# Optimization experiments

Measured on AMD Instinct MI355X. Metric: run time of the kernel, lower is better.

## Reference

```python
import jax, jax.numpy as jnp
import numpy as np

HEADS = 8


def setup_inputs() -> dict:
    key = jax.random.key(0)
    ks = jax.random.split(key, 6)
    B, N, D = 4, 2048, 512
    return {
        "x": jax.random.normal(ks[0], (B, N, D), dtype=jnp.float32),
        "pos": jax.random.uniform(ks[1], (B, N, 3), dtype=jnp.float32),
        "qkv_w": jax.random.normal(ks[2], (3 * D, D), dtype=jnp.float32) * 0.02,
        "qkv_b": jax.random.normal(ks[3], (3 * D,), dtype=jnp.float32) * 0.02,
        "out_w": jax.random.normal(ks[4], (D, D), dtype=jnp.float32) * 0.02,
        "out_b": jax.random.normal(ks[5], (D,), dtype=jnp.float32) * 0.02,
    }


def reference(x, pos, qkv_w, qkv_b, out_w, out_b):
    B, N, D = x.shape
    H = HEADS
    Dh = D // H
    scale = D ** (-0.5)  # NOTE: original uses full dim, not head dim

    # QKV projection -> [3, B, H, N, Dh]
    qkv = (x @ qkv_w.T + qkv_b).reshape(B, N, 3, H, Dh).transpose(2, 0, 3, 1, 4)
    q, k, v = qkv[0], qkv[1], qkv[2]

    # partial 3D RoPE on first 6 head dims (3 axis pairs)
    theta = pos * jnp.pi                    # [B, N, 3]
    sin = jnp.sin(theta)[:, None]           # [B, 1, N, 3] broadcasts over heads
    cos = jnp.cos(theta)[:, None]

    def rotate(t):
        x_rot = t[..., :6]
        x1 = x_rot[..., 0::2]               # [B, H, N, 3]
        x2 = x_rot[..., 1::2]
        return jnp.concatenate(
            [x1 * cos - x2 * sin, x1 * sin + x2 * cos, t[..., 6:]], axis=-1
        )

    q = rotate(q)
    k = rotate(k)

    attn = jax.nn.softmax(jnp.einsum("bhqd,bhkd->bhqk", q, k) * scale, axis=-1)
    out = jnp.einsum("bhqk,bhkd->bhqd", attn, v)          # [B, H, N, Dh]
    out = out.transpose(0, 2, 1, 3).reshape(B, N, D)
    return out @ out_w.T + out_b
```

## Files before the change

### kernel.cpp

```cpp
#include <hip/hip_runtime.h>
#include <stdint.h>

typedef __attribute__((ext_vector_type(4))) float f32x4;
typedef __attribute__((ext_vector_type(16))) float f32x16;
typedef __attribute__((ext_vector_type(8))) short bf16x8;
typedef __attribute__((ext_vector_type(4))) unsigned short u16x4;

__device__ __forceinline__ unsigned short f2bf(float f) {
    unsigned int u = __builtin_bit_cast(unsigned int, f);
    u += 0x7fffu + ((u >> 16) & 1u);
    return (unsigned short)(u >> 16);
}
__device__ __forceinline__ float bf2f(unsigned short s) {
    unsigned int u = ((unsigned int)s) << 16;
    return __builtin_bit_cast(float, u);
}
__device__ __forceinline__ float fexp2(float x) {
#if __has_builtin(__builtin_amdgcn_exp2f)
    return __builtin_amdgcn_exp2f(x);
#else
    return exp2f(x);
#endif
}
__device__ __forceinline__ unsigned int cvt_pk_bf16(float lo, float hi) {
    unsigned int r;
    asm("v_cvt_pk_bf16_f32 %0, %1, %2" : "=v"(r) : "v"(lo), "v"(hi));
    return r;
}

__global__ void k_cvt3(const float* __restrict__ x,
                       const float* __restrict__ w1,
                       const float* __restrict__ w2,
                       unsigned short* __restrict__ out) {
    const int C1 = 1048576;
    const int C2 = 196608;
    int i = blockIdx.x * blockDim.x + threadIdx.x;
    f32x4 v;
    if (i < C1)            v = ((const f32x4*)x)[i];
    else if (i < C1 + C2)  v = ((const f32x4*)w1)[i - C1];
    else                   v = ((const f32x4*)w2)[i - C1 - C2];
    u16x4 o;
    o.x = f2bf(v.x); o.y = f2bf(v.y); o.z = f2bf(v.z); o.w = f2bf(v.w);
    ((u16x4*)out)[i] = o;
}

template<int OUT_BF16>
__global__ __launch_bounds__(256, 2)
void k_gemm_nt(const unsigned short* __restrict__ A,
               const unsigned short* __restrict__ Bm,
               const float* __restrict__ bias,
               void* __restrict__ Cout, int M, int N, int K) {
    __shared__ unsigned short As[2][128 * 64];
    __shared__ unsigned short Bs[2][128 * 64];
    const int tid = threadIdx.x;
    const int lane = tid & 63;
    const int w = tid >> 6;
    const int wr = (w >> 1) * 64, wc = (w & 1) * 64;
    const int g = lane >> 4, fr = lane & 15;

    f32x4 acc[4][4];
#pragma unroll
    for (int i = 0; i < 4; ++i)
#pragma unroll
        for (int j = 0; j < 4; ++j) acc[i][j] = f32x4{0.f, 0.f, 0.f, 0.f};

    const int srow8 = lane >> 3;
    const int swc = ((lane & 7) ^ srow8) * 8;
    const unsigned short* Abase = A + (size_t)(blockIdx.x * 128 + w * 8 + srow8) * K + swc;
    const unsigned short* Bbase = Bm + (size_t)(blockIdx.y * 128 + w * 8 + srow8) * K + swc;

    auto stage = [&](int bsel, int k0) {
        char* ldsA = (char*)&As[bsel][0] + w * 1024;
        char* ldsB = (char*)&Bs[bsel][0] + w * 1024;
#pragma unroll
        for (int i = 0; i < 4; ++i) {
            __builtin_amdgcn_global_load_lds(
                (const __attribute__((address_space(1))) void*)(Abase + (size_t)i * 32 * K + k0),
                (__attribute__((address_space(3))) void*)(ldsA + i * 4096), 16, 0, 0);
            __builtin_amdgcn_global_load_lds(
                (const __attribute__((address_space(1))) void*)(Bbase + (size_t)i * 32 * K + k0),
                (__attribute__((address_space(3))) void*)(ldsB + i * 4096), 16, 0, 0);
        }
    };
    auto compute = [&](int bsel) {
        bf16x8 af[2][4], bfv[2][4];
#pragma unroll
        for (int kk = 0; kk < 2; ++kk) {
#pragma unroll
            for (int mi = 0; mi < 4; ++mi)
                af[kk][mi] = *(const bf16x8*)&As[bsel][(wr + mi * 16 + fr) * 64 + (((kk * 4 + g) ^ (fr & 7)) * 8)];
#pragma unroll
            for (int ni = 0; ni < 4; ++ni)
                bfv[kk][ni] = *(const bf16x8*)&Bs[bsel][(wc + ni * 16 + fr) * 64 + (((kk * 4 + g) ^ (fr & 7)) * 8)];
        }
        __builtin_amdgcn_s_setprio(1);
#pragma unroll
        for (int kk = 0; kk < 2; ++kk)
#pragma unroll
            for (int mi = 0; mi < 4; ++mi)
#pragma unroll
                for (int ni = 0; ni < 4; ++ni)
                    acc[mi][ni] = __builtin_amdgcn_mfma_f32_16x16x32_bf16(af[kk][mi], bfv[kk][ni], acc[mi][ni], 0, 0, 0);
        __builtin_amdgcn_s_setprio(0);
    };

    const int nt = K >> 6;
    stage(0, 0);
    int cur = 0;
#pragma unroll 1
    for (int t = 0; t < nt - 1; ++t) {
        __builtin_amdgcn_s_barrier();
        stage(cur ^ 1, (t + 1) << 6);
        asm volatile("s_waitcnt vmcnt(8)" ::: "memory");
        __builtin_amdgcn_s_barrier();
        compute(cur);
        cur ^= 1;
    }
    asm volatile("s_waitcnt vmcnt(0)" ::: "memory");
    __builtin_amdgcn_s_barrier();
    compute(cur);

#pragma unroll
    for (int mi = 0; mi < 4; ++mi) {
#pragma unroll
        for (int ni = 0; ni < 4; ++ni) {
            int row = blockIdx.x * 128 + wr + mi * 16 + g * 4;
            int col = blockIdx.y * 128 + wc + ni * 16 + fr;
            float bz = bias[col];
#pragma unroll
            for (int r = 0; r < 4; ++r) {
                float v = acc[mi][ni][r] + bz;
                if (OUT_BF16) ((unsigned short*)Cout)[(size_t)(row + r) * N + col] = f2bf(v);
                else          ((float*)Cout)[(size_t)(row + r) * N + col] = v;
            }
        }
    }
}

__global__ void k_rotary(const unsigned short* __restrict__ qkv,
                         const float* __restrict__ pos,
                         unsigned short* __restrict__ Qb,
                         unsigned short* __restrict__ Kb,
                         unsigned short* __restrict__ VT) {
    const float PI = 3.14159265358979323846f;
    const float QS = 0.04419417382415922f * 1.44269504088896341f;
    int cid = blockIdx.x * 256 + threadIdx.x;
    int s = cid >> 19;
    int r = cid & 524287;
    if (s < 2) {
        int m = r >> 6, c = r & 63;
        int h = c >> 3, dc = c & 7;
        int b = m >> 11, n = m & 2047;
        bf16x8 v = *(const bf16x8*)&qkv[m * 1536 + s * 512 + c * 8];
        float f[8];
#pragma unroll
        for (int i = 0; i < 8; ++i) f[i] = bf2f((unsigned short)v[i]);
        if (dc == 0) {
            float nf[6];
#pragma unroll
            for (int j = 0; j < 3; ++j) {
                float th = pos[m * 3 + j] * PI;
                float sn = __sinf(th), cs = __cosf(th);
                float x1 = f[2 * j], x2 = f[2 * j + 1];
                nf[j] = x1 * cs - x2 * sn;
                nf[3 + j] = x1 * sn + x2 * cs;
            }
#pragma unroll
            for (int j = 0; j < 6; ++j) f[j] = nf[j];
        }
        if (s == 0) {
#pragma unroll
            for (int i = 0; i < 8; ++i) f[i] *= QS;
        }
        bf16x8 o;
#pragma unroll
        for (int i = 0; i < 8; ++i) o[i] = (short)f2bf(f[i]);
        unsigned short* dst = (s == 0) ? Qb : Kb;
        *(bf16x8*)&dst[((size_t)(b * 8 + h) * 2048 + n) * 64 + dc * 8] = o;
    } else {
        int cd = r >> 13;
        int m = r & 8191;
        int b = m >> 11, n = m & 2047;
        int h = cd >> 3, d8 = (cd & 7) * 8;
        bf16x8 v = *(const bf16x8*)&qkv[m * 1536 + 1024 + cd * 8];
        int q2 = (n >> 2) & 3;
        int np = n + (q2 == 1 ? 4 : (q2 == 2 ? -4 : 0));
        size_t base = ((size_t)(b * 8 + h) * 64 + d8) * 2048 + np;
#pragma unroll
        for (int i = 0; i < 8; ++i) VT[base + (size_t)i * 2048] = (unsigned short)v[i];
    }
}

__global__ __launch_bounds__(512, 4)
void k_attn(const unsigned short* __restrict__ Qb,
            const unsigned short* __restrict__ Kb,
            const unsigned short* __restrict__ VT,
            unsigned short* __restrict__ Ob) {
    __shared__ unsigned short smem[2][2][2][4096];
    const int tid = threadIdx.x, lane = tid & 63, w = tid >> 6;
    const int wl = w & 3, half = w >> 2;
    const int l31 = lane & 31, hi = lane >> 5;
    const int bid = blockIdx.x;
    const int bh = (bid & 7) * 4 + ((bid >> 3) >> 4);
    const int qb = (bid >> 3) & 15;
    const int b = bh >> 3, h = bh & 7;
    const int qr0 = qb * 128 + wl * 32;
    const unsigned short* Q = Qb + (size_t)bh * 2048 * 64;
    const unsigned short* K = Kb + (size_t)bh * 2048 * 64;
    const unsigned short* V = VT + (size_t)bh * 64 * 2048;
    const int thalf = half * 16;

    const int srow8 = lane >> 3;
    const int swc = ((lane & 7) ^ srow8) << 3;
    const int sA = wl, sB = wl + 4;

    bf16x8 bq[4];
#pragma unroll
    for (int ds = 0; ds < 4; ++ds)
        bq[ds] = *(const bf16x8*)&Q[(size_t)(qr0 + l31) * 64 + ds * 16 + hi * 8];

    f32x16 oT0, oT1;
#pragma unroll
    for (int i = 0; i < 16; ++i) { oT0[i] = 0.f; oT1[i] = 0.f; }
    float lpart = 0.f;

    auto stage = [&](int bsel, int t) {
        const int kv0 = t * 64;
        const unsigned short* k0 = K + (size_t)(kv0 + sA * 8 + srow8) * 64 + swc;
        const unsigned short* k1 = K + (size_t)(kv0 + sB * 8 + srow8) * 64 + swc;
        const unsigned short* v0 = V + (size_t)(sA * 8 + srow8) * 2048 + kv0 + swc;
        const unsigned short* v1 = V + (size_t)(sB * 8 + srow8) * 2048 + kv0 + swc;
        char* dk = (char*)&smem[half][0][bsel][0];
        char* dv = (char*)&smem[half][1][bsel][0];
        __builtin_amdgcn_global_load_lds((const __attribute__((address_space(1))) void*)k0,
                                         (__attribute__((address_space(3))) void*)(dk + sA * 1024), 16, 0, 0);
        __builtin_amdgcn_global_load_lds((const __attribute__((address_space(1))) void*)k1,
                                         (__attribute__((address_space(3))) void*)(dk + sB * 1024), 16, 0, 0);
        __builtin_amdgcn_global_load_lds((const __attribute__((address_space(1))) void*)v0,
                                         (__attribute__((address_space(3))) void*)(dv + sA * 1024), 16, 0, 0);
        __builtin_amdgcn_global_load_lds((const __attribute__((address_space(1))) void*)v1,
                                         (__attribute__((address_space(3))) void*)(dv + sB * 1024), 16, 0, 0);
    };

    auto pack8 = [&](const float* p) -> bf16x8 {
        union { unsigned int u[4]; bf16x8 v; } c;
        c.u[0] = cvt_pk_bf16(p[0], p[1]);
        c.u[1] = cvt_pk_bf16(p[2], p[3]);
        c.u[2] = cvt_pk_bf16(p[4], p[5]);
        c.u[3] = cvt_pk_bf16(p[6], p[7]);
        return c.v;
    };

    auto compute = [&](int bsel) {
        const unsigned short* KsC = &smem[half][0][bsel][0];
        const unsigned short* VtC = &smem[half][1][bsel][0];
        f32x16 s0, s1;
#pragma unroll
        for (int i = 0; i < 16; ++i) { s0[i] = 0.f; s1[i] = 0.f; }
        __builtin_amdgcn_s_setprio(1);
#pragma unroll
        for (int ds = 0; ds < 4; ++ds) {
            const int c = ((((ds << 1) | hi) ^ (l31 & 7)) << 3);
            bf16x8 ka0 = *(const bf16x8*)&KsC[l31 * 64 + c];
            bf16x8 ka1 = *(const bf16x8*)&KsC[(32 + l31) * 64 + c];
            s0 = __builtin_amdgcn_mfma_f32_32x32x16_bf16(ka0, bq[ds], s0, 0, 0, 0);
            s1 = __builtin_amdgcn_mfma_f32_32x32x16_bf16(ka1, bq[ds], s1, 0, 0, 0);
        }
        __builtin_amdgcn_s_setprio(0);
        float p0[16], p1[16];
        float lsum = 0.f;
#pragma unroll
        for (int r = 0; r < 16; ++r) {
            p0[r] = fexp2(s0[r]);
            p1[r] = fexp2(s1[r]);
            lsum += p0[r] + p1[r];
        }
        lpart += lsum;
        bf16x8 pb0 = pack8(p0);
        bf16x8 pb1 = pack8(p0 + 8);
        bf16x8 pb2 = pack8(p1);
        bf16x8 pb3 = pack8(p1 + 8);
        __builtin_amdgcn_s_setprio(1);
#pragma unroll
        for (int kb = 0; kb < 4; ++kb) {
            const int c = ((((kb << 1) | hi) ^ (l31 & 7)) << 3);
            bf16x8 av0 = *(const bf16x8*)&VtC[l31 * 64 + c];
            bf16x8 av1 = *(const bf16x8*)&VtC[(32 + l31) * 64 + c];
            bf16x8 pbk = (kb == 0) ? pb0 : (kb == 1) ? pb1 : (kb == 2) ? pb2 : pb3;
            oT0 = __builtin_amdgcn_mfma_f32_32x32x16_bf16(av0, pbk, oT0, 0, 0, 0);
            oT1 = __builtin_amdgcn_mfma_f32_32x32x16_bf16(av1, pbk, oT1, 0, 0, 0);
        }
        __builtin_amdgcn_s_setprio(0);
    };

    stage(0, thalf);
    int cur = 0;
#pragma unroll 1
    for (int t = 0; t < 15; ++t) {
        __builtin_amdgcn_s_barrier();
        stage(cur ^ 1, thalf + t + 1);
        asm volatile("s_waitcnt vmcnt(4)" ::: "memory");
        __builtin_amdgcn_s_barrier();
        compute(cur);
        cur ^= 1;
    }
    asm volatile("s_waitcnt vmcnt(0)" ::: "memory");
    __builtin_amdgcn_s_barrier();
    compute(cur);

    __syncthreads();
    float* mrg = (float*)&smem[0][0][0][0];
    float* slot = mrg + (size_t)(wl * 64 + lane) * 33;
    if (half) {
#pragma unroll
        for (int i = 0; i < 16; ++i) { slot[i] = oT0[i]; slot[16 + i] = oT1[i]; }
        slot[32] = lpart;
    }
    __syncthreads();
    if (!half) {
#pragma unroll
        for (int i = 0; i < 16; ++i) { oT0[i] += slot[i]; oT1[i] += slot[16 + i]; }
        float lf = lpart + slot[32];
        lf += __shfl_xor(lf, 32, 64);
        float il = 1.f / lf;
        size_t rowbase = (size_t)(b * 2048 + qr0 + l31) * 512 + h * 64;
#pragma unroll
        for (int grp = 0; grp < 4; ++grp) {
            u16x4 o0, o1;
#pragma unroll
            for (int i = 0; i < 4; ++i) {
                o0[i] = f2bf(oT0[grp * 4 + i] * il);
                o1[i] = f2bf(oT1[grp * 4 + i] * il);
            }
            int dv0 = grp * 8 + 4 * hi;
            *(u16x4*)&Ob[rowbase + dv0] = o0;
            *(u16x4*)&Ob[rowbase + 32 + dv0] = o1;
        }
    }
}

extern "C" void kernel_launch(void* const* d_in, const int* in_sizes, int n_in,
                              void* d_out, int out_size, void* d_ws, size_t ws_size,
                              hipStream_t stream) {
    const float* x     = (const float*)d_in[0];
    const float* pos   = (const float*)d_in[1];
    const float* qkv_w = (const float*)d_in[2];
    const float* qkv_b = (const float*)d_in[3];
    const float* out_w = (const float*)d_in[4];
    const float* out_b = (const float*)d_in[5];
    float* out = (float*)d_out;

    unsigned short* Xb   = (unsigned short*)d_ws;
    unsigned short* W1b  = Xb   + (size_t)8192 * 512;
    unsigned short* W2b  = W1b  + (size_t)1536 * 512;
    unsigned short* QKVb = W2b  + (size_t)512 * 512;
    unsigned short* Qb   = QKVb + (size_t)8192 * 1536;
    unsigned short* Kb   = Qb   + (size_t)4194304;
    unsigned short* VTb  = Kb   + (size_t)4194304;
    unsigned short* Ob   = VTb  + (size_t)4194304;

    k_cvt3<<<5120, 256, 0, stream>>>(x, qkv_w, out_w, Xb);
    k_gemm_nt<1><<<dim3(64, 12), 256, 0, stream>>>(Xb, W1b, qkv_b, QKVb, 8192, 1536, 512);
    k_rotary<<<6144, 256, 0, stream>>>(QKVb, pos, Qb, Kb, VTb);
    k_attn<<<512, 512, 0, stream>>>(Qb, Kb, VTb, Ob);
    k_gemm_nt<0><<<dim3(64, 4), 256, 0, stream>>>(Ob, W2b, out_b, out, 8192, 512, 512);
}
```

Baseline: 96.03 us.

## Restructure GEMM and attention pipelines to one barrier per step with smaller K tiles

The GEMM kernel halves its K tile from 64 to 32, shrinking LDS buffers and using a 4-chunk XOR swizzle. Both the GEMM and attention loops move from a two-barrier-per-iteration scheme, which waited on loads before computing, to a single barrier per step. The next tile is issued, the current one is computed, and only then does the loop wait and synchronize, so loads overlap a full compute step. The trade-off is more loop iterations and barriers per K, with less MFMA work between them.

```diff
diff --git a/kernel.cpp b/kernel.cpp
--- a/kernel.cpp
+++ b/kernel.cpp
@@ -50,8 +50,8 @@
                const unsigned short* __restrict__ Bm,
                const float* __restrict__ bias,
                void* __restrict__ Cout, int M, int N, int K) {
-    __shared__ unsigned short As[2][128 * 64];
-    __shared__ unsigned short Bs[2][128 * 64];
+    __shared__ unsigned short As[2][128 * 32];
+    __shared__ unsigned short Bs[2][128 * 32];
     const int tid = threadIdx.x;
     const int lane = tid & 63;
     const int w = tid >> 6;
@@ -64,61 +64,59 @@
 #pragma unroll
         for (int j = 0; j < 4; ++j) acc[i][j] = f32x4{0.f, 0.f, 0.f, 0.f};
 
-    const int srow8 = lane >> 3;
-    const int swc = ((lane & 7) ^ srow8) * 8;
-    const unsigned short* Abase = A + (size_t)(blockIdx.x * 128 + w * 8 + srow8) * K + swc;
-    const unsigned short* Bbase = Bm + (size_t)(blockIdx.y * 128 + w * 8 + srow8) * K + swc;
+    const int srow16 = lane >> 2;
+    const int schunk = ((lane & 3) ^ (srow16 & 3)) * 8;
+    const int sA = w, sB = w + 4;
+    const unsigned short* Aseg0 = A + (size_t)(blockIdx.x * 128 + sA * 16 + srow16) * K + schunk;
+    const unsigned short* Aseg1 = A + (size_t)(blockIdx.x * 128 + sB * 16 + srow16) * K + schunk;
+    const unsigned short* Bseg0 = Bm + (size_t)(blockIdx.y * 128 + sA * 16 + srow16) * K + schunk;
+    const unsigned short* Bseg1 = Bm + (size_t)(blockIdx.y * 128 + sB * 16 + srow16) * K + schunk;
 
     auto stage = [&](int bsel, int k0) {
-        char* ldsA = (char*)&As[bsel][0] + w * 1024;
-        char* ldsB = (char*)&Bs[bsel][0] + w * 1024;
-#pragma unroll
-        for (int i = 0; i < 4; ++i) {
-            __builtin_amdgcn_global_load_lds(
-                (const __attribute__((address_space(1))) void*)(Abase + (size_t)i * 32 * K + k0),
-                (__attribute__((address_space(3))) void*)(ldsA + i * 4096), 16, 0, 0);
-            __builtin_amdgcn_global_load_lds(
-                (const __attribute__((address_space(1))) void*)(Bbase + (size_t)i * 32 * K + k0),
-                (__attribute__((address_space(3))) void*)(ldsB + i * 4096), 16, 0, 0);
-        }
+        char* la = (char*)&As[bsel][0];
+        char* lb = (char*)&Bs[bsel][0];
+        __builtin_amdgcn_global_load_lds((const __attribute__((address_space(1))) void*)(Aseg0 + k0),
+                                         (__attribute__((address_space(3))) void*)(la + sA * 1024), 16, 0, 0);
+        __builtin_amdgcn_global_load_lds((const __attribute__((address_space(1))) void*)(Aseg1 + k0),
+                                         (__attribute__((address_space(3))) void*)(la + sB * 1024), 16, 0, 0);
+        __builtin_amdgcn_global_load_lds((const __attribute__((address_space(1))) void*)(Bseg0 + k0),
+                                         (__attribute__((address_space(3))) void*)(lb + sA * 1024), 16, 0, 0);
+        __builtin_amdgcn_global_load_lds((const __attribute__((address_space(1))) void*)(Bseg1 + k0),
+                                         (__attribute__((address_space(3))) void*)(lb + sB * 1024), 16, 0, 0);
     };
     auto compute = [&](int bsel) {
-        bf16x8 af[2][4], bfv[2][4];
-#pragma unroll
-        for (int kk = 0; kk < 2; ++kk) {
-#pragma unroll
-            for (int mi = 0; mi < 4; ++mi)
-                af[kk][mi] = *(const bf16x8*)&As[bsel][(wr + mi * 16 + fr) * 64 + (((kk * 4 + g) ^ (fr & 7)) * 8)];
+        bf16x8 af[4], bfv[4];
+        const int rc = (g ^ (fr & 3)) * 8;
+#pragma unroll
+        for (int mi = 0; mi < 4; ++mi)
+            af[mi] = *(const bf16x8*)&As[bsel][(wr + mi * 16 + fr) * 32 + rc];
+#pragma unroll
+        for (int ni = 0; ni < 4; ++ni)
+            bfv[ni] = *(const bf16x8*)&Bs[bsel][(wc + ni * 16 + fr) * 32 + rc];
+        __builtin_amdgcn_s_setprio(1);
+#pragma unroll
+        for (int mi = 0; mi < 4; ++mi)
 #pragma unroll
             for (int ni = 0; ni < 4; ++ni)
-                bfv[kk][ni] = *(const bf16x8*)&Bs[bsel][(wc + ni * 16 + fr) * 64 + (((kk * 4 + g) ^ (fr & 7)) * 8)];
-        }
-        __builtin_amdgcn_s_setprio(1);
-#pragma unroll
-        for (int kk = 0; kk < 2; ++kk)
-#pragma unroll
-            for (int mi = 0; mi < 4; ++mi)
-#pragma unroll
-                for (int ni = 0; ni < 4; ++ni)
-                    acc[mi][ni] = __builtin_amdgcn_mfma_f32_16x16x32_bf16(af[kk][mi], bfv[kk][ni], acc[mi][ni], 0, 0, 0);
+                acc[mi][ni] = __builtin_amdgcn_mfma_f32_16x16x32_bf16(af[mi], bfv[ni], acc[mi][ni], 0, 0, 0);
         __builtin_amdgcn_s_setprio(0);
     };
 
-    const int nt = K >> 6;
+    const int nt = K >> 5;
     stage(0, 0);
+    asm volatile("s_waitcnt vmcnt(0)" ::: "memory");
+    __builtin_amdgcn_s_barrier();
     int cur = 0;
 #pragma unroll 1
-    for (int t = 0; t < nt - 1; ++t) {
-        __builtin_amdgcn_s_barrier();
-        stage(cur ^ 1, (t + 1) << 6);
-        asm volatile("s_waitcnt vmcnt(8)" ::: "memory");
-        __builtin_amdgcn_s_barrier();
+    for (int t = 0; t < nt; ++t) {
+        if (t < nt - 1) stage(cur ^ 1, (t + 1) << 5);
         compute(cur);
+        if (t < nt - 1) {
+            asm volatile("s_waitcnt vmcnt(0)" ::: "memory");
+            __builtin_amdgcn_s_barrier();
+        }
         cur ^= 1;
     }
-    asm volatile("s_waitcnt vmcnt(0)" ::: "memory");
-    __builtin_amdgcn_s_barrier();
-    compute(cur);
 
 #pragma unroll
     for (int mi = 0; mi < 4; ++mi) {
@@ -294,19 +292,19 @@
     };
 
     stage(0, thalf);
+    asm volatile("s_waitcnt vmcnt(0)" ::: "memory");
+    __builtin_amdgcn_s_barrier();
     int cur = 0;
 #pragma unroll 1
-    for (int t = 0; t < 15; ++t) {
-        __builtin_amdgcn_s_barrier();
-        stage(cur ^ 1, thalf + t + 1);
-        asm volatile("s_waitcnt vmcnt(4)" ::: "memory");
-        __builtin_amdgcn_s_barrier();
+    for (int t = 0; t < 16; ++t) {
+        if (t < 15) stage(cur ^ 1, thalf + t + 1);
         compute(cur);
+        if (t < 15) {
+            asm volatile("s_waitcnt vmcnt(0)" ::: "memory");
+            __builtin_amdgcn_s_barrier();
+        }
         cur ^= 1;
     }
-    asm volatile("s_waitcnt vmcnt(0)" ::: "memory");
-    __builtin_amdgcn_s_barrier();
-    compute(cur);
 
     __syncthreads();
     float* mrg = (float*)&smem[0][0][0][0];
```

Result: no change. 94.75 us (-1.3%).
